# Kernel optimization log

Hardware: AMD Instinct MI355X
Metric: run time of the kernel (lower is better)

The kernel has to match this reference:

```python
import jax, jax.numpy as jnp
import numpy as np

K = 16          # number of discrete value bins (values in [0, K))
EPOCHS = 200.0  # self.epochs in the module


def _mi_from_joint(joint):
    # sklearn mutual_info_score from a KxK contingency table (natural log)
    n = joint.sum()
    pij = joint / n
    pi = pij.sum(axis=1, keepdims=True)
    pj = pij.sum(axis=0, keepdims=True)
    safe_log = lambda p: jnp.log(jnp.where(p > 0, p, 1.0))
    terms = pij * (safe_log(pij) - safe_log(pi) - safe_log(pj))
    return jnp.where(pij > 0, terms, 0.0).sum()


def _pair_mi(a, b):
    # a, b: int32 vectors of equal length; histogram-based MI
    idx = a * K + b
    joint = jnp.zeros(K * K, jnp.float32).at[idx].add(1.0).reshape(K, K)
    return _mi_from_joint(joint)


def _mi_mask(x):
    # x: (b, t, c, h, w) float with integer values in [0, K)
    b, t, c, h, w = x.shape
    s = x.astype(jnp.int32).transpose(1, 0, 2, 3, 4).reshape(t, b * c, h * w)
    s0 = s[0]
    # global MI between t=0 and each t, over all b*c*h*w samples
    glob = jax.vmap(lambda st: _pair_mi(s0.reshape(-1), st.reshape(-1)))(s)  # (t,)
    # per-spatial-element MI between t=0 and each t, over b*c samples
    ele = jax.vmap(jax.vmap(_pair_mi, in_axes=(1, 1)), in_axes=(None, 0))(s0, s)  # (t, hw)
    mi = ele * glob[:, None]
    mi = mi / mi[0]          # divide every row by row 0 (broadcast over t)
    mi = mi.at[0].set(0.0)
    return mi.reshape(t, h, w)


def setup_inputs() -> dict:
    key = jax.random.key(0)
    k1, k2 = jax.random.split(key)
    b, t, c, h, w = 16, 8, 32, 64, 64
    x = jax.random.randint(k1, (b, t, c, h, w), 0, K).astype(jnp.float32)
    noise = jax.random.uniform(k2, (b, t, c, h, w), dtype=jnp.float32)
    return {"x": x, "noise": noise, "epoch": 50}


def reference(x, noise, epoch):
    mi = _mi_mask(x)                                   # (t, h, w)
    prob = jnp.clip(mi * (epoch / EPOCHS), 0.0, 1.0)
    mask = noise < prob[None, :, None, :, :]           # (b,t,c,h,w)
    return jnp.where(mask, 0.0, x)
```

## Files before the change

### kernel.cpp

```cpp
#include <hip/hip_runtime.h>
#include <math.h>

#define B_   16
#define T_   8
#define C_   32
#define HW_  4096
#define K_   16
#define BC_  (B_*C_)
#define P_BLK 8

typedef unsigned int uint;

__device__ __forceinline__ int rot2_(int t, int lp) { return 37 * lp + 13 * t; }

__global__ __launch_bounds__(256) void k_pack(const float4* __restrict__ x4,
                                              uint4* __restrict__ packed4,
                                              uint4* __restrict__ glob_hist4) {
  const int tid = threadIdx.x;
  if (blockIdx.x == 0) {
    const uint4 z = make_uint4(0u, 0u, 0u, 0u);
    glob_hist4[tid] = z;
    glob_hist4[tid + 256] = z;
  }
  const int n  = blockIdx.x * 256 + tid;
  const int bc = n >> 10;
  const int p4 = n & 1023;
  const int b  = bc >> 5;
  const int c  = bc & 31;
  uint4 acc = make_uint4(0u, 0u, 0u, 0u);
  #pragma unroll
  for (int t = 0; t < T_; ++t) {
    const float4 xv = x4[((b * T_ + t) * C_ + c) * (HW_ / 4) + p4];
    const int sh = 4 * t;
    acc.x |= ((uint)xv.x) << sh;
    acc.y |= ((uint)xv.y) << sh;
    acc.z |= ((uint)xv.z) << sh;
    acc.w |= ((uint)xv.w) << sh;
  }
  packed4[n] = acc;
}

__global__ __launch_bounds__(512, 8) void k_hist_mi(const uint* __restrict__ packed,
                                                    uint* __restrict__ glob_hist,
                                                    double* __restrict__ ele) {
  __shared__ uint   histw[T_][P_BLK][128];
  __shared__ double logtab[513];

  const int tid = threadIdx.x;
  const int p0  = blockIdx.x * P_BLK;

  for (int i = tid; i < T_ * P_BLK * 128; i += 512) ((uint*)histw)[i] = 0u;
  for (int i = tid; i < 513; i += 512) logtab[i] = (i > 0) ? log((double)i) : 0.0;
  __syncthreads();

  const int lp = tid & 7;
  const int g  = tid >> 3;

  uint w[8];
  #pragma unroll
  for (int k = 0; k < 8; ++k)
    w[k] = packed[(g + (k << 6)) * HW_ + p0 + lp];

  #pragma unroll
  for (int k = 0; k < 8; ++k) {
    const uint wk  = w[k];
    const int  a   = (int)(wk & 15u);
    const int  row = a << 4;
    {
      const int rb = ((row | a) + rot2_(0, lp)) & 255;
      atomicAdd(&histw[0][lp][rb >> 1], 1u << ((rb & 1) << 4));
    }
    #pragma unroll
    for (int t = 1; t < T_; ++t) {
      const int v  = (int)((wk >> (4 * t)) & 15u);
      const int rb = ((row | v) + rot2_(t, lp)) & 255;
      atomicAdd(&histw[t][lp][rb >> 1], 1u << ((rb & 1) << 4));
    }
  }
  __syncthreads();

  for (int i = tid; i < T_ * 256; i += 512) {
    const int t = i >> 8, bin = i & 255;
    uint s = 0;
    #pragma unroll
    for (int p = 0; p < P_BLK; ++p) {
      const int rb = (bin + rot2_(t, p)) & 255;
      s += (histw[t][p][rb >> 1] >> ((rb & 1) << 4)) & 0xffffu;
    }
    atomicAdd(&glob_hist[i], s);
  }

  if (tid < T_ * P_BLK) {
    const int t   = tid >> 3;
    const int lpp = tid & 7;
    const int rr  = rot2_(t, lpp);
    const uint* h = &histw[t][lpp][0];
    double term = 0.0;
    uint col[K_];
    #pragma unroll
    for (int v = 0; v < K_; ++v) col[v] = 0u;
    #pragma unroll
    for (int a = 0; a < K_; ++a) {
      uint r = 0;
      #pragma unroll
      for (int v = 0; v < K_; ++v) {
        const int  rb  = (((a << 4) | v) + rr) & 255;
        const uint cnt = (h[rb >> 1] >> ((rb & 1) << 4)) & 0xffffu;
        r += cnt;
        col[v] += cnt;
        term += (double)cnt * logtab[cnt];
      }
      term -= (double)r * logtab[r];
    }
    #pragma unroll
    for (int v = 0; v < K_; ++v)
      term -= (double)col[v] * logtab[col[v]];
    ele[t * HW_ + p0 + lpp] = logtab[512] + term * (1.0 / 512.0);
  }
}

__global__ __launch_bounds__(256) void k_glob_prob(const uint* __restrict__ glob_hist,
                                                   const double* __restrict__ ele,
                                                   const int* __restrict__ epoch_ptr,
                                                   float* __restrict__ prob) {
  __shared__ double part[256];
  __shared__ double glob[T_];
  const int tid = threadIdx.x;

  if (tid < 128) {
    const int t = tid >> 4, a = tid & 15;
    const uint* h = glob_hist + t * 256 + (a << 4);
    double s = 0.0, r = 0.0;
    #pragma unroll
    for (int v = 0; v < K_; ++v) {
      const double cnt = (double)h[v];
      r += cnt;
      if (cnt > 0.0) s += cnt * log(cnt);
    }
    if (r > 0.0) s -= r * log(r);
    part[tid] = s;
  } else {
    const int t = (tid - 128) >> 4, v = (tid - 128) & 15;
    const uint* h = glob_hist + t * 256 + v;
    double col = 0.0;
    #pragma unroll
    for (int a = 0; a < K_; ++a) col += (double)h[a << 4];
    part[tid] = (col > 0.0) ? -col * log(col) : 0.0;
  }
  __syncthreads();

  if (tid < T_) {
    double term = 0.0;
    #pragma unroll
    for (int i = 0; i < 16; ++i)
      term += part[tid * 16 + i] + part[128 + tid * 16 + i];
    const double n = (double)BC_ * (double)HW_;
    glob[tid] = log(n) + term / n;
  }
  __syncthreads();

  const double escale = (double)(*epoch_ptr) * (1.0 / 200.0);
  #pragma unroll
  for (int k = 0; k < 4; ++k) {
    const int i = blockIdx.x * 1024 + k * 256 + tid;
    const int t = i >> 12;
    const int p = i & (HW_ - 1);
    float pv = 0.0f;
    if (t != 0) {
      const double mi0 = ele[p] * glob[0];
      const double mit = ele[i] * glob[t];
      const double v  = (mit / mi0) * escale;
      pv = fminf(fmaxf((float)v, 0.0f), 1.0f);
    }
    prob[i] = pv;
  }
}

__global__ __launch_bounds__(256) void k_mask(const uint4* __restrict__ packed4,
                                              const float4* __restrict__ n4,
                                              const float* __restrict__ prob,
                                              float4* __restrict__ o4) {
  const int i  = blockIdx.x * 256 + threadIdx.x;
  const int p4 = i & 1023;
  const int tc = i >> 10;
  const int c  = tc & 31;
  const int bt = tc >> 5;
  const int t  = bt & 7;
  const int b  = bt >> 3;
  const uint4 pk = packed4[(((b << 5) | c) << 10) | p4];
  const int sh = 4 * t;
  float4 xv;
  xv.x = (float)((pk.x >> sh) & 15u);
  xv.y = (float)((pk.y >> sh) & 15u);
  xv.z = (float)((pk.z >> sh) & 15u);
  xv.w = (float)((pk.w >> sh) & 15u);
  const float4 pr = ((const float4*)prob)[(t << 10) | p4];
  const float4 nv = n4[i];
  float4 o;
  o.x = (nv.x < pr.x) ? 0.0f : xv.x;
  o.y = (nv.y < pr.y) ? 0.0f : xv.y;
  o.z = (nv.z < pr.z) ? 0.0f : xv.z;
  o.w = (nv.w < pr.w) ? 0.0f : xv.w;
  o4[i] = o;
}

extern "C" void kernel_launch(void* const* d_in, const int* in_sizes, int n_in,
                              void* d_out, int out_size, void* d_ws, size_t ws_size,
                              hipStream_t stream) {
  const float* x     = (const float*)d_in[0];
  const float* noise = (const float*)d_in[1];
  const int*   epoch = (const int*)d_in[2];
  float*       out   = (float*)d_out;

  char* ws = (char*)d_ws;
  uint*   glob_hist = (uint*)ws;
  uint*   packed    = (uint*)(ws + 8192);
  double* ele       = (double*)(ws + 8192 + (size_t)BC_ * HW_ * 4);
  float*  prob      = (float*)((char*)ele + (size_t)T_ * HW_ * 8);

  k_pack<<<(BC_ * HW_ / 4) / 256, 256, 0, stream>>>((const float4*)x,
                                                    (uint4*)packed,
                                                    (uint4*)glob_hist);
  k_hist_mi<<<HW_ / P_BLK, 512, 0, stream>>>(packed, glob_hist, ele);
  k_glob_prob<<<32, 256, 0, stream>>>(glob_hist, ele, epoch, prob);

  const int n4 = (B_ * T_ * C_ * HW_) / 4;
  k_mask<<<n4 / 256, 256, 0, stream>>>((const uint4*)packed,
                                       (const float4*)noise,
                                       prob, (float4*)out);
}
```

Measured before the change: 211.9 us.

## Write transposed packed copy so histogram kernel reads coalesced per-pixel rows

The pack kernel now stages a 64x64 tile of packed words in shared memory and also writes a transposed copy laid out as pixel-major over b*c. The histogram kernel reads this transposed buffer, so each group of threads loads contiguous words instead of strided 32-byte-sparse accesses. The cost is an extra 8 MB write plus a shared-memory transpose and fewer, larger pack blocks (512 instead of 2048).

New measurement: 211.9 us. No clear change (+0.0%).

```diff
diff --git a/kernel.cpp b/kernel.cpp
--- a/kernel.cpp
+++ b/kernel.cpp
@@ -15,32 +15,60 @@
 
 __global__ __launch_bounds__(256) void k_pack(const float4* __restrict__ x4,
                                               uint4* __restrict__ packed4,
+                                              uint4* __restrict__ packedT4,
                                               uint4* __restrict__ glob_hist4) {
+  __shared__ uint tile[64][65];
   const int tid = threadIdx.x;
   if (blockIdx.x == 0) {
     const uint4 z = make_uint4(0u, 0u, 0u, 0u);
     glob_hist4[tid] = z;
     glob_hist4[tid + 256] = z;
   }
-  const int n  = blockIdx.x * 256 + tid;
-  const int bc = n >> 10;
-  const int p4 = n & 1023;
-  const int b  = bc >> 5;
-  const int c  = bc & 31;
-  uint4 acc = make_uint4(0u, 0u, 0u, 0u);
-  #pragma unroll
-  for (int t = 0; t < T_; ++t) {
-    const float4 xv = x4[((b * T_ + t) * C_ + c) * (HW_ / 4) + p4];
-    const int sh = 4 * t;
-    acc.x |= ((uint)xv.x) << sh;
-    acc.y |= ((uint)xv.y) << sh;
-    acc.z |= ((uint)xv.z) << sh;
-    acc.w |= ((uint)xv.w) << sh;
-  }
-  packed4[n] = acc;
-}
-
-__global__ __launch_bounds__(512, 8) void k_hist_mi(const uint* __restrict__ packed,
+  const int bc0 = (blockIdx.x & 7) * 64;
+  const int pC  = blockIdx.x >> 3;
+  const int p40 = pC * 16;
+
+  #pragma unroll
+  for (int j = 0; j < 4; ++j) {
+    const int idx  = j * 256 + tid;
+    const int bc_l = idx >> 4;
+    const int p4   = idx & 15;
+    const int bc   = bc0 + bc_l;
+    const int b    = bc >> 5, c = bc & 31;
+    uint4 acc = make_uint4(0u, 0u, 0u, 0u);
+    #pragma unroll
+    for (int t = 0; t < T_; ++t) {
+      const float4 xv = x4[((b * T_ + t) * C_ + c) * (HW_ / 4) + p40 + p4];
+      const int sh = 4 * t;
+      acc.x |= ((uint)xv.x) << sh;
+      acc.y |= ((uint)xv.y) << sh;
+      acc.z |= ((uint)xv.z) << sh;
+      acc.w |= ((uint)xv.w) << sh;
+    }
+    packed4[bc * (HW_ / 4) + p40 + p4] = acc;
+    const int pl = p4 << 2;
+    tile[bc_l][pl + 0] = acc.x;
+    tile[bc_l][pl + 1] = acc.y;
+    tile[bc_l][pl + 2] = acc.z;
+    tile[bc_l][pl + 3] = acc.w;
+  }
+  __syncthreads();
+
+  #pragma unroll
+  for (int j = 0; j < 4; ++j) {
+    const int idx = j * 256 + tid;
+    const int p_l = idx >> 4;
+    const int bc4 = idx & 15;
+    uint4 v;
+    v.x = tile[(bc4 << 2) + 0][p_l];
+    v.y = tile[(bc4 << 2) + 1][p_l];
+    v.z = tile[(bc4 << 2) + 2][p_l];
+    v.w = tile[(bc4 << 2) + 3][p_l];
+    packedT4[(pC * 64 + p_l) * (BC_ / 4) + (bc0 >> 2) + bc4] = v;
+  }
+}
+
+__global__ __launch_bounds__(512, 8) void k_hist_mi(const uint* __restrict__ packedT,
                                                     uint* __restrict__ glob_hist,
                                                     double* __restrict__ ele) {
   __shared__ uint   histw[T_][P_BLK][128];
@@ -53,13 +81,13 @@
   for (int i = tid; i < 513; i += 512) logtab[i] = (i > 0) ? log((double)i) : 0.0;
   __syncthreads();
 
-  const int lp = tid & 7;
-  const int g  = tid >> 3;
+  const int lp = tid >> 6;
+  const int g  = tid & 63;
 
   uint w[8];
   #pragma unroll
   for (int k = 0; k < 8; ++k)
-    w[k] = packed[(g + (k << 6)) * HW_ + p0 + lp];
+    w[k] = packedT[(p0 + lp) * BC_ + (k << 6) + g];
 
   #pragma unroll
   for (int k = 0; k < 8; ++k) {
@@ -213,15 +241,16 @@
   float*       out   = (float*)d_out;
 
   char* ws = (char*)d_ws;
+  const size_t packed_bytes = (size_t)BC_ * HW_ * 4;
   uint*   glob_hist = (uint*)ws;
   uint*   packed    = (uint*)(ws + 8192);
-  double* ele       = (double*)(ws + 8192 + (size_t)BC_ * HW_ * 4);
+  uint*   packedT   = (uint*)(ws + 8192 + packed_bytes);
+  double* ele       = (double*)(ws + 8192 + 2 * packed_bytes);
   float*  prob      = (float*)((char*)ele + (size_t)T_ * HW_ * 8);
 
-  k_pack<<<(BC_ * HW_ / 4) / 256, 256, 0, stream>>>((const float4*)x,
-                                                    (uint4*)packed,
-                                                    (uint4*)glob_hist);
-  k_hist_mi<<<HW_ / P_BLK, 512, 0, stream>>>(packed, glob_hist, ele);
+  k_pack<<<512, 256, 0, stream>>>((const float4*)x, (uint4*)packed,
+                                  (uint4*)packedT, (uint4*)glob_hist);
+  k_hist_mi<<<HW_ / P_BLK, 512, 0, stream>>>(packedT, glob_hist, ele);
   k_glob_prob<<<32, 256, 0, stream>>>(glob_hist, ele, epoch, prob);
 
   const int n4 = (B_ * T_ * C_ * HW_) / 4;
```
